# Kernel tuning notes

Measured on AMD Instinct MI355X. Metric: run time of the kernel, lower is better.

## Reference

```python
import jax, jax.numpy as jnp
import numpy as np

FRAME_LEN = 512
FRAME_HOP = 256
EPSILON = float(np.finfo(np.float32).eps)


def _dft_kernels(frame_len=FRAME_LEN):
    # Matches torch: K = view_as_real(fft.rfft(eye(N), dim=1))[:frame_len], windowed by hann.
    # rfft of delta at t gives exp(-2pi i f t / N): real = cos, imag = -sin.
    N = frame_len  # already a power of two
    n = jnp.arange(frame_len, dtype=jnp.float32)
    window = 0.5 * (1.0 - jnp.cos(2.0 * jnp.pi * n / frame_len))  # periodic hann
    f = jnp.arange(N // 2 + 1, dtype=jnp.float32)  # 257 bins
    ang = 2.0 * jnp.pi * f[:, None] * n[None, :] / N  # [F, L]
    Kr = jnp.cos(ang) * window
    Ki = -jnp.sin(ang) * window  # torch rfft imaginary part
    return Kr, Ki


def _frame(x, frame_len=FRAME_LEN, hop=FRAME_HOP):
    B, Ns = x.shape
    T = (Ns - frame_len) // hop + 1
    idx = jnp.arange(T)[:, None] * hop + jnp.arange(frame_len)[None, :]  # [T, L]
    return x[:, idx]  # [B, T, L]


def reference(x):
    Kr, Ki = _dft_kernels()
    xf = _frame(x)  # [B, T, L]
    r = jnp.einsum('btl,fl->bft', xf, Kr)       # real part of conv1d output
    i = -jnp.einsum('btl,fl->bft', xf, Ki)      # i = -imag (as in torch code)
    mag = jnp.sqrt(r * r + i * i)               # B x F x T
    f = jnp.clip(mag, EPSILON, None)
    mean = jnp.mean(f, axis=-1, keepdims=True)
    std = jnp.std(f, axis=-1, keepdims=True, ddof=1)  # torch std is unbiased
    feat = (f - mean) / (std + EPSILON)
    return mag, feat


def setup_inputs() -> dict:
    key = jax.random.key(0)
    x = jax.random.normal(key, (64, 160000), dtype=jnp.float32)
    return {"x": x}
```

## Files before the change

kernel.cpp:

```cpp
#include <hip/hip_runtime.h>
#include <math.h>

#define FRAME_LEN 512
#define HOP       256
#define NFREQ     257
#define NFREQ_PAD 288
#define NBATCH    64
#define NSAMP     160000
#define TFRAMES   624
#define EPS       1.1920928955078125e-07f

#define MT 128
#define FT 32
#define BK 64
#define NK (FRAME_LEN / BK)
#define NXCD 8
#define XBLKS 5000

typedef __attribute__((ext_vector_type(8))) short short8;
typedef __attribute__((ext_vector_type(4))) float f32x4;

static __device__ __forceinline__ unsigned int f2bf(float f) {
    unsigned int u = __float_as_uint(f);
    return (u + 0x7fffu + ((u >> 16) & 1u)) >> 16;
}
static __device__ __forceinline__ uint4 pack8(float4 a, float4 b) {
    uint4 r;
    r.x = f2bf(a.x) | (f2bf(a.y) << 16);
    r.y = f2bf(a.z) | (f2bf(a.w) << 16);
    r.z = f2bf(b.x) | (f2bf(b.y) << 16);
    r.w = f2bf(b.z) | (f2bf(b.w) << 16);
    return r;
}
static __device__ __forceinline__ void gload_lds16(const void* g, void* l) {
    __builtin_amdgcn_global_load_lds(
        (const __attribute__((address_space(1))) void*)g,
        (__attribute__((address_space(3))) void*)l, 16, 0, 0);
}

__global__ __launch_bounds__(256) void prep(const float* __restrict__ x,
                                            unsigned short* __restrict__ xbf,
                                            unsigned short* __restrict__ Wc,
                                            unsigned short* __restrict__ Ws) {
    if (blockIdx.x < XBLKS) {
        int i = blockIdx.x * 256 + threadIdx.x;
        const float4* src = (const float4*)x + (size_t)i * 2;
        float4 a = src[0], b = src[1];
        *(uint4*)(xbf + (size_t)i * 8) = pack8(a, b);
    } else {
        int f = blockIdx.x - XBLKS;
        for (int n = threadIdx.x; n < FRAME_LEN; n += 256) {
            unsigned short c = 0, s = 0;
            if (f < NFREQ) {
                float w = 0.5f * (1.0f - cosf(2.0f * (float)M_PI * (float)n / (float)FRAME_LEN));
                int r = (f * n) & (FRAME_LEN - 1);
                float ang = (float)r * (2.0f * (float)M_PI / (float)FRAME_LEN);
                float sv, cv;
                sincosf(ang, &sv, &cv);
                c = (unsigned short)f2bf(cv * w);
                s = (unsigned short)f2bf(sv * w);
            }
            Wc[f * FRAME_LEN + n] = c;
            Ws[f * FRAME_LEN + n] = s;
        }
    }
}

__global__ __launch_bounds__(256) void stft_mfma(
    const unsigned short* __restrict__ xbf, const unsigned short* __restrict__ Wc,
    const unsigned short* __restrict__ Ws, float* __restrict__ mag)
{
    __shared__ unsigned short As[2][MT][BK];
    __shared__ unsigned short Bs[2][2][FT][BK];

    const int tid = threadIdx.x;
    const int logical = (blockIdx.x % NXCD) * (2808 / NXCD) + blockIdx.x / NXCD;
    const int tileM = logical / 9;
    const int tileF = logical % 9;
    const int wid = tid >> 6;
    const int lane = tid & 63;
    const int lrow = lane & 15;
    const int lhi = lane >> 4;

    const unsigned short* pA[4];
    #pragma unroll
    for (int j = 0; j < 4; j++) {
        int idx = wid * 4 + j;
        int row = idx * 8 + (lane >> 3);
        int m = tileM * MT + row;
        int b = m / TFRAMES;
        int t = m - b * TFRAMES;
        int chunk = (lane & 7) ^ (row & 7);
        pA[j] = xbf + (size_t)b * NSAMP + t * HOP + chunk * 8;
    }
    const unsigned short* pB[2];
    #pragma unroll
    for (int j = 0; j < 2; j++) {
        int i = wid * 2 + j;
        int row = (i & 3) * 8 + (lane >> 3);
        int f = tileF * FT + row;
        int chunk = (lane & 7) ^ (row & 7);
        const unsigned short* tbl = (i & 4) ? Ws : Wc;
        pB[j] = tbl + f * FRAME_LEN + chunk * 8;
    }

    f32x4 accr[2][2] = {};
    f32x4 acci[2][2] = {};

    #pragma unroll
    for (int j = 0; j < 4; j++)
        gload_lds16(pA[j], (unsigned short*)As[0] + (wid * 4 + j) * 512);
    #pragma unroll
    for (int j = 0; j < 2; j++)
        gload_lds16(pB[j], (unsigned short*)Bs[0] + (wid * 2 + j) * 512);
    __syncthreads();

    for (int it = 0; it < NK; it++) {
        const int cur = it & 1;
        if (it < NK - 1) {
            const int k0 = (it + 1) * BK;
            #pragma unroll
            for (int j = 0; j < 4; j++)
                gload_lds16(pA[j] + k0, (unsigned short*)As[cur ^ 1] + (wid * 4 + j) * 512);
            #pragma unroll
            for (int j = 0; j < 2; j++)
                gload_lds16(pB[j] + k0, (unsigned short*)Bs[cur ^ 1] + (wid * 2 + j) * 512);
        }
        #pragma unroll
        for (int ks = 0; ks < 2; ks++) {
            short8 a[2], bc[2], bsn[2];
            const int c = (ks * 4 + lhi) ^ (lrow & 7);
            #pragma unroll
            for (int mf = 0; mf < 2; mf++)
                a[mf] = *(const short8*)&As[cur][wid * 32 + mf * 16 + lrow][c * 8];
            #pragma unroll
            for (int nf = 0; nf < 2; nf++) {
                bc[nf]  = *(const short8*)&Bs[cur][0][nf * 16 + lrow][c * 8];
                bsn[nf] = *(const short8*)&Bs[cur][1][nf * 16 + lrow][c * 8];
            }
            #pragma unroll
            for (int mf = 0; mf < 2; mf++) {
                #pragma unroll
                for (int nf = 0; nf < 2; nf++) {
                    accr[mf][nf] = __builtin_amdgcn_mfma_f32_16x16x32_bf16(
                        a[mf], bc[nf], accr[mf][nf], 0, 0, 0);
                    acci[mf][nf] = __builtin_amdgcn_mfma_f32_16x16x32_bf16(
                        a[mf], bsn[nf], acci[mf][nf], 0, 0, 0);
                }
            }
        }
        __syncthreads();
    }

    #pragma unroll
    for (int mf = 0; mf < 2; mf++) {
        int m0 = tileM * MT + wid * 32 + mf * 16 + lhi * 4;
        int b = m0 / TFRAMES;
        int t = m0 - b * TFRAMES;
        #pragma unroll
        for (int nf = 0; nf < 2; nf++) {
            int f = tileF * FT + nf * 16 + lrow;
            if (f < NFREQ) {
                float4 o;
                o.x = sqrtf(accr[mf][nf][0] * accr[mf][nf][0] + acci[mf][nf][0] * acci[mf][nf][0]);
                o.y = sqrtf(accr[mf][nf][1] * accr[mf][nf][1] + acci[mf][nf][1] * acci[mf][nf][1]);
                o.z = sqrtf(accr[mf][nf][2] * accr[mf][nf][2] + acci[mf][nf][2] * acci[mf][nf][2]);
                o.w = sqrtf(accr[mf][nf][3] * accr[mf][nf][3] + acci[mf][nf][3] * acci[mf][nf][3]);
                *(float4*)(mag + ((size_t)b * NFREQ + f) * TFRAMES + t) = o;
            }
        }
    }
}

__global__ __launch_bounds__(256) void normalize(const float* __restrict__ mag,
                                                 float* __restrict__ feat)
{
    const int row = blockIdx.x * 4 + (threadIdx.x >> 6);
    const int lane = threadIdx.x & 63;
    const float* mp = mag + (size_t)row * TFRAMES;

    float4 v[3];
    float sum = 0.f;
    #pragma unroll
    for (int i = 0; i < 3; i++) {
        int c4 = lane + i * 64;
        if (c4 < TFRAMES / 4) {
            float4 t = *(const float4*)(mp + c4 * 4);
            t.x = fmaxf(t.x, EPS); t.y = fmaxf(t.y, EPS);
            t.z = fmaxf(t.z, EPS); t.w = fmaxf(t.w, EPS);
            v[i] = t;
            sum += (t.x + t.y) + (t.z + t.w);
        } else {
            v[i] = make_float4(0.f, 0.f, 0.f, 0.f);
        }
    }
    #pragma unroll
    for (int off = 1; off < 64; off <<= 1) sum += __shfl_xor(sum, off, 64);
    const float mean = sum * (1.0f / (float)TFRAMES);

    float ssd = 0.f;
    #pragma unroll
    for (int i = 0; i < 3; i++) {
        int c4 = lane + i * 64;
        if (c4 < TFRAMES / 4) {
            float dx = v[i].x - mean, dy = v[i].y - mean;
            float dz = v[i].z - mean, dw = v[i].w - mean;
            ssd += (dx * dx + dy * dy) + (dz * dz + dw * dw);
        }
    }
    #pragma unroll
    for (int off = 1; off < 64; off <<= 1) ssd += __shfl_xor(ssd, off, 64);
    const float stdv = sqrtf(ssd * (1.0f / (float)(TFRAMES - 1)));
    const float inv = 1.0f / (stdv + EPS);

    float* fp = feat + (size_t)row * TFRAMES;
    #pragma unroll
    for (int i = 0; i < 3; i++) {
        int c4 = lane + i * 64;
        if (c4 < TFRAMES / 4) {
            float4 o;
            o.x = (v[i].x - mean) * inv; o.y = (v[i].y - mean) * inv;
            o.z = (v[i].z - mean) * inv; o.w = (v[i].w - mean) * inv;
            *(float4*)(fp + c4 * 4) = o;
        }
    }
}

extern "C" void kernel_launch(void* const* d_in, const int* in_sizes, int n_in,
                              void* d_out, int out_size, void* d_ws, size_t ws_size,
                              hipStream_t stream) {
    const float* x = (const float*)d_in[0];
    unsigned short* Wc  = (unsigned short*)d_ws;
    unsigned short* Ws  = Wc + NFREQ_PAD * FRAME_LEN;
    unsigned short* xbf = Ws + NFREQ_PAD * FRAME_LEN;
    float* mag  = (float*)d_out;
    float* feat = mag + (size_t)NBATCH * NFREQ * TFRAMES;

    prep<<<XBLKS + NFREQ_PAD, 256, 0, stream>>>(x, xbf, Wc, Ws);

    stft_mfma<<<312 * 9, 256, 0, stream>>>(xbf, Wc, Ws, mag);

    normalize<<<NBATCH * NFREQ / 4, 256, 0, stream>>>(mag, feat);
}
```

Before: 61.49 us.

## Fuse STFT magnitude GEMM with per-row normalization using register-stashed values

```diff
diff --git a/kernel.cpp b/kernel.cpp
--- a/kernel.cpp
+++ b/kernel.cpp
@@ -9,13 +9,7 @@
 #define NSAMP     160000
 #define TFRAMES   624
 #define EPS       1.1920928955078125e-07f
-
-#define MT 128
-#define FT 32
-#define BK 64
-#define NK (FRAME_LEN / BK)
-#define NXCD 8
-#define XBLKS 5000
+#define XBLKS     5000
 
 typedef __attribute__((ext_vector_type(8))) short short8;
 typedef __attribute__((ext_vector_type(4))) float f32x4;
@@ -23,6 +17,12 @@
 static __device__ __forceinline__ unsigned int f2bf(float f) {
     unsigned int u = __float_as_uint(f);
     return (u + 0x7fffu + ((u >> 16) & 1u)) >> 16;
+}
+static __device__ __forceinline__ float bf2f_lo(unsigned int p) {
+    return __uint_as_float(p << 16);
+}
+static __device__ __forceinline__ float bf2f_hi(unsigned int p) {
+    return __uint_as_float(p & 0xffff0000u);
 }
 static __device__ __forceinline__ uint4 pack8(float4 a, float4 b) {
     uint4 r;
@@ -66,162 +66,169 @@
     }
 }
 
-__global__ __launch_bounds__(256) void stft_mfma(
-    const unsigned short* __restrict__ xbf, const unsigned short* __restrict__ Wc,
-    const unsigned short* __restrict__ Ws, float* __restrict__ mag)
+static __device__ __forceinline__ void stage(
+    unsigned short* AsB, unsigned short* BsB, int buf, int p, int c,
+    const unsigned short* xb, const unsigned short* Wc, const unsigned short* Ws,
+    int ftile, int tid)
 {
-    __shared__ unsigned short As[2][MT][BK];
-    __shared__ unsigned short Bs[2][2][FT][BK];
-
-    const int tid = threadIdx.x;
-    const int logical = (blockIdx.x % NXCD) * (2808 / NXCD) + blockIdx.x / NXCD;
-    const int tileM = logical / 9;
-    const int tileF = logical % 9;
-    const int wid = tid >> 6;
-    const int lane = tid & 63;
-    const int lrow = lane & 15;
-    const int lhi = lane >> 4;
-
-    const unsigned short* pA[4];
-    #pragma unroll
-    for (int j = 0; j < 4; j++) {
-        int idx = wid * 4 + j;
-        int row = idx * 8 + (lane >> 3);
-        int m = tileM * MT + row;
-        int b = m / TFRAMES;
-        int t = m - b * TFRAMES;
-        int chunk = (lane & 7) ^ (row & 7);
-        pA[j] = xbf + (size_t)b * NSAMP + t * HOP + chunk * 8;
-    }
-    const unsigned short* pB[2];
-    #pragma unroll
-    for (int j = 0; j < 2; j++) {
-        int i = wid * 2 + j;
-        int row = (i & 3) * 8 + (lane >> 3);
-        int f = tileF * FT + row;
-        int chunk = (lane & 7) ^ (row & 7);
-        const unsigned short* tbl = (i & 4) ? Ws : Wc;
-        pB[j] = tbl + f * FRAME_LEN + chunk * 8;
-    }
-
-    f32x4 accr[2][2] = {};
-    f32x4 acci[2][2] = {};
-
+    const int k0 = c * 32;
+    int t = p * 256 + tid;
+    if (t > TFRAMES - 1) t = TFRAMES - 1;
+    const unsigned short* srcA = xb + t * HOP + k0;
     #pragma unroll
     for (int j = 0; j < 4; j++)
-        gload_lds16(pA[j], (unsigned short*)As[0] + (wid * 4 + j) * 512);
-    #pragma unroll
-    for (int j = 0; j < 2; j++)
-        gload_lds16(pB[j], (unsigned short*)Bs[0] + (wid * 2 + j) * 512);
-    __syncthreads();
-
-    for (int it = 0; it < NK; it++) {
-        const int cur = it & 1;
-        if (it < NK - 1) {
-            const int k0 = (it + 1) * BK;
-            #pragma unroll
-            for (int j = 0; j < 4; j++)
-                gload_lds16(pA[j] + k0, (unsigned short*)As[cur ^ 1] + (wid * 4 + j) * 512);
-            #pragma unroll
-            for (int j = 0; j < 2; j++)
-                gload_lds16(pB[j] + k0, (unsigned short*)Bs[cur ^ 1] + (wid * 2 + j) * 512);
-        }
-        #pragma unroll
-        for (int ks = 0; ks < 2; ks++) {
-            short8 a[2], bc[2], bsn[2];
-            const int c = (ks * 4 + lhi) ^ (lrow & 7);
-            #pragma unroll
-            for (int mf = 0; mf < 2; mf++)
-                a[mf] = *(const short8*)&As[cur][wid * 32 + mf * 16 + lrow][c * 8];
+        gload_lds16(srcA + j * 8, AsB + buf * 8192 + j * 2048 + tid * 8);
+    const unsigned short* tb = (tid < 128) ? Wc : Ws;
+    const int bf = ftile * 32 + (tid & 31);
+    const int ch = (tid & 127) >> 5;
+    gload_lds16(tb + bf * 512 + k0 + ch * 8, BsB + buf * 2048 + tid * 8);
+}
+
+template<int P, int MF, int WS>
+static __device__ __forceinline__ void do_pass(
+    int& buf, unsigned short* AsB, unsigned short* BsB,
+    const unsigned short* xb, const unsigned short* Wc, const unsigned short* Ws,
+    int ftile, int tid, int wid, int lrow, int lhi, int b,
+    float* __restrict__ mag, float* ssum, float* ssq,
+    unsigned int stash[10][2][2])
+{
+    f32x4 ar[MF][2] = {};
+    f32x4 ai[MF][2] = {};
+    #pragma unroll
+    for (int c = 0; c < 16; c++) {
+        const int nit = P * 16 + c + 1;
+        if (nit < 48)
+            stage(AsB, BsB, buf ^ 1, nit >> 4, nit & 15, xb, Wc, Ws, ftile, tid);
+        short8 av[MF], bcv[2], bsv[2];
+        #pragma unroll
+        for (int mf = 0; mf < MF; mf++)
+            av[mf] = *(const short8*)(AsB + buf * 8192 + lhi * 2048 +
+                                      (wid * WS + mf * 16 + lrow) * 8);
+        #pragma unroll
+        for (int nf = 0; nf < 2; nf++) {
+            bcv[nf] = *(const short8*)(BsB + buf * 2048 + lhi * 256 + (nf * 16 + lrow) * 8);
+            bsv[nf] = *(const short8*)(BsB + buf * 2048 + 1024 + lhi * 256 + (nf * 16 + lrow) * 8);
+        }
+        #pragma unroll
+        for (int mf = 0; mf < MF; mf++) {
             #pragma unroll
             for (int nf = 0; nf < 2; nf++) {
-                bc[nf]  = *(const short8*)&Bs[cur][0][nf * 16 + lrow][c * 8];
-                bsn[nf] = *(const short8*)&Bs[cur][1][nf * 16 + lrow][c * 8];
-            }
+                ar[mf][nf] = __builtin_amdgcn_mfma_f32_16x16x32_bf16(
+                    av[mf], bcv[nf], ar[mf][nf], 0, 0, 0);
+                ai[mf][nf] = __builtin_amdgcn_mfma_f32_16x16x32_bf16(
+                    av[mf], bsv[nf], ai[mf][nf], 0, 0, 0);
+            }
+        }
+        __syncthreads();
+        buf ^= 1;
+    }
+    #pragma unroll
+    for (int mf = 0; mf < MF; mf++) {
+        const int tile = (P < 2) ? (P * 16 + wid * 4 + mf) : (32 + wid * 2 + mf);
+        const int t = tile * 16 + lhi * 4;
+        const bool tv = (tile < 39);
+        #pragma unroll
+        for (int nf = 0; nf < 2; nf++) {
+            const int f = ftile * 32 + nf * 16 + lrow;
+            const float m0 = sqrtf(ar[mf][nf][0] * ar[mf][nf][0] + ai[mf][nf][0] * ai[mf][nf][0]);
+            const float m1 = sqrtf(ar[mf][nf][1] * ar[mf][nf][1] + ai[mf][nf][1] * ai[mf][nf][1]);
+            const float m2 = sqrtf(ar[mf][nf][2] * ar[mf][nf][2] + ai[mf][nf][2] * ai[mf][nf][2]);
+            const float m3 = sqrtf(ar[mf][nf][3] * ar[mf][nf][3] + ai[mf][nf][3] * ai[mf][nf][3]);
+            if (tv && f < NFREQ) {
+                float4 o = make_float4(m0, m1, m2, m3);
+                *(float4*)(mag + ((size_t)b * NFREQ + f) * TFRAMES + t) = o;
+            }
+            const float c0 = fmaxf(m0, EPS), c1 = fmaxf(m1, EPS);
+            const float c2 = fmaxf(m2, EPS), c3 = fmaxf(m3, EPS);
+            if (tv) {
+                ssum[nf] += (c0 + c1) + (c2 + c3);
+                ssq[nf]  += (c0 * c0 + c1 * c1) + (c2 * c2 + c3 * c3);
+            }
+            const int si = (P < 2) ? (P * 4 + mf) : (8 + mf);
+            stash[si][nf][0] = f2bf(c0) | (f2bf(c1) << 16);
+            stash[si][nf][1] = f2bf(c2) | (f2bf(c3) << 16);
+        }
+    }
+}
+
+__global__ __launch_bounds__(256) void stft_fused(
+    const unsigned short* __restrict__ xbf, const unsigned short* __restrict__ Wc,
+    const unsigned short* __restrict__ Ws, float* __restrict__ mag,
+    float* __restrict__ feat)
+{
+    __shared__ unsigned short As[2][4][256][8];
+    __shared__ unsigned short Bs[2][2][4][32][8];
+    const int tid = threadIdx.x;
+    const int logical = ((int)blockIdx.x & 7) * 72 + ((int)blockIdx.x >> 3);
+    const int b = logical / 9;
+    const int ftile = logical - b * 9;
+    const int wid = tid >> 6, lane = tid & 63, lrow = lane & 15, lhi = lane >> 4;
+    const unsigned short* xb = xbf + (size_t)b * NSAMP;
+    unsigned short* AsB = &As[0][0][0][0];
+    unsigned short* BsB = &Bs[0][0][0][0][0];
+
+    float ssum[2] = {0.f, 0.f}, ssq[2] = {0.f, 0.f};
+    unsigned int stash[10][2][2];
+
+    stage(AsB, BsB, 0, 0, 0, xb, Wc, Ws, ftile, tid);
+    __syncthreads();
+    int buf = 0;
+    do_pass<0, 4, 64>(buf, AsB, BsB, xb, Wc, Ws, ftile, tid, wid, lrow, lhi, b, mag, ssum, ssq, stash);
+    do_pass<1, 4, 64>(buf, AsB, BsB, xb, Wc, Ws, ftile, tid, wid, lrow, lhi, b, mag, ssum, ssq, stash);
+    do_pass<2, 2, 32>(buf, AsB, BsB, xb, Wc, Ws, ftile, tid, wid, lrow, lhi, b, mag, ssum, ssq, stash);
+
+    #pragma unroll
+    for (int nf = 0; nf < 2; nf++) {
+        ssum[nf] += __shfl_xor(ssum[nf], 16, 64);
+        ssum[nf] += __shfl_xor(ssum[nf], 32, 64);
+        ssq[nf]  += __shfl_xor(ssq[nf], 16, 64);
+        ssq[nf]  += __shfl_xor(ssq[nf], 32, 64);
+    }
+    float* red = (float*)AsB;
+    if (lane < 16) {
+        #pragma unroll
+        for (int nf = 0; nf < 2; nf++) {
+            red[((wid * 2 + nf) * 16 + lane) * 2 + 0] = ssum[nf];
+            red[((wid * 2 + nf) * 16 + lane) * 2 + 1] = ssq[nf];
+        }
+    }
+    __syncthreads();
+    float mean[2], inv[2];
+    #pragma unroll
+    for (int nf = 0; nf < 2; nf++) {
+        float S = 0.f, Q = 0.f;
+        #pragma unroll
+        for (int w = 0; w < 4; w++) {
+            S += red[((w * 2 + nf) * 16 + lrow) * 2 + 0];
+            Q += red[((w * 2 + nf) * 16 + lrow) * 2 + 1];
+        }
+        const float mu = S * (1.0f / (float)TFRAMES);
+        float var = (Q - (float)TFRAMES * mu * mu) * (1.0f / (float)(TFRAMES - 1));
+        var = fmaxf(var, 0.f);
+        mean[nf] = mu;
+        inv[nf] = 1.0f / (sqrtf(var) + EPS);
+    }
+    #pragma unroll
+    for (int si = 0; si < 10; si++) {
+        const int tile = (si < 8) ? ((si >> 2) * 16 + wid * 4 + (si & 3))
+                                  : (32 + wid * 2 + (si - 8));
+        const int t = tile * 16 + lhi * 4;
+        if (tile < 39) {
             #pragma unroll
-            for (int mf = 0; mf < 2; mf++) {
-                #pragma unroll
-                for (int nf = 0; nf < 2; nf++) {
-                    accr[mf][nf] = __builtin_amdgcn_mfma_f32_16x16x32_bf16(
-                        a[mf], bc[nf], accr[mf][nf], 0, 0, 0);
-                    acci[mf][nf] = __builtin_amdgcn_mfma_f32_16x16x32_bf16(
-                        a[mf], bsn[nf], acci[mf][nf], 0, 0, 0);
+            for (int nf = 0; nf < 2; nf++) {
+                const int f = ftile * 32 + nf * 16 + lrow;
+                if (f < NFREQ) {
+                    const float c0 = bf2f_lo(stash[si][nf][0]);
+                    const float c1 = bf2f_hi(stash[si][nf][0]);
+                    const float c2 = bf2f_lo(stash[si][nf][1]);
+                    const float c3 = bf2f_hi(stash[si][nf][1]);
+                    float4 o = make_float4((c0 - mean[nf]) * inv[nf],
+                                           (c1 - mean[nf]) * inv[nf],
+                                           (c2 - mean[nf]) * inv[nf],
+                                           (c3 - mean[nf]) * inv[nf]);
+                    *(float4*)(feat + ((size_t)b * NFREQ + f) * TFRAMES + t) = o;
                 }
             }
-        }
-        __syncthreads();
-    }
-
-    #pragma unroll
-    for (int mf = 0; mf < 2; mf++) {
-        int m0 = tileM * MT + wid * 32 + mf * 16 + lhi * 4;
-        int b = m0 / TFRAMES;
-        int t = m0 - b * TFRAMES;
-        #pragma unroll
-        for (int nf = 0; nf < 2; nf++) {
-            int f = tileF * FT + nf * 16 + lrow;
-            if (f < NFREQ) {
-                float4 o;
-                o.x = sqrtf(accr[mf][nf][0] * accr[mf][nf][0] + acci[mf][nf][0] * acci[mf][nf][0]);
-                o.y = sqrtf(accr[mf][nf][1] * accr[mf][nf][1] + acci[mf][nf][1] * acci[mf][nf][1]);
-                o.z = sqrtf(accr[mf][nf][2] * accr[mf][nf][2] + acci[mf][nf][2] * acci[mf][nf][2]);
-                o.w = sqrtf(accr[mf][nf][3] * accr[mf][nf][3] + acci[mf][nf][3] * acci[mf][nf][3]);
-                *(float4*)(mag + ((size_t)b * NFREQ + f) * TFRAMES + t) = o;
-            }
-        }
-    }
-}
-
-__global__ __launch_bounds__(256) void normalize(const float* __restrict__ mag,
-                                                 float* __restrict__ feat)
-{
-    const int row = blockIdx.x * 4 + (threadIdx.x >> 6);
-    const int lane = threadIdx.x & 63;
-    const float* mp = mag + (size_t)row * TFRAMES;
-
-    float4 v[3];
-    float sum = 0.f;
-    #pragma unroll
-    for (int i = 0; i < 3; i++) {
-        int c4 = lane + i * 64;
-        if (c4 < TFRAMES / 4) {
-            float4 t = *(const float4*)(mp + c4 * 4);
-            t.x = fmaxf(t.x, EPS); t.y = fmaxf(t.y, EPS);
-            t.z = fmaxf(t.z, EPS); t.w = fmaxf(t.w, EPS);
-            v[i] = t;
-            sum += (t.x + t.y) + (t.z + t.w);
-        } else {
-            v[i] = make_float4(0.f, 0.f, 0.f, 0.f);
-        }
-    }
-    #pragma unroll
-    for (int off = 1; off < 64; off <<= 1) sum += __shfl_xor(sum, off, 64);
-    const float mean = sum * (1.0f / (float)TFRAMES);
-
-    float ssd = 0.f;
-    #pragma unroll
-    for (int i = 0; i < 3; i++) {
-        int c4 = lane + i * 64;
-        if (c4 < TFRAMES / 4) {
-            float dx = v[i].x - mean, dy = v[i].y - mean;
-            float dz = v[i].z - mean, dw = v[i].w - mean;
-            ssd += (dx * dx + dy * dy) + (dz * dz + dw * dw);
-        }
-    }
-    #pragma unroll
-    for (int off = 1; off < 64; off <<= 1) ssd += __shfl_xor(ssd, off, 64);
-    const float stdv = sqrtf(ssd * (1.0f / (float)(TFRAMES - 1)));
-    const float inv = 1.0f / (stdv + EPS);
-
-    float* fp = feat + (size_t)row * TFRAMES;
-    #pragma unroll
-    for (int i = 0; i < 3; i++) {
-        int c4 = lane + i * 64;
-        if (c4 < TFRAMES / 4) {
-            float4 o;
-            o.x = (v[i].x - mean) * inv; o.y = (v[i].y - mean) * inv;
-            o.z = (v[i].z - mean) * inv; o.w = (v[i].w - mean) * inv;
-            *(float4*)(fp + c4 * 4) = o;
         }
     }
 }
@@ -238,7 +245,5 @@
 
     prep<<<XBLKS + NFREQ_PAD, 256, 0, stream>>>(x, xbf, Wc, Ws);
 
-    stft_mfma<<<312 * 9, 256, 0, stream>>>(xbf, Wc, Ws, mag);
-
-    normalize<<<NBATCH * NFREQ / 4, 256, 0, stream>>>(mag, feat);
-}
+    stft_fused<<<NBATCH * 9, 256, 0, stream>>>(xbf, Wc, Ws, mag, feat);
+}
```

Result: slower. 122.2 us (+98.8%).

## Triple-buffer LDS tiles with partial vmcnt waits in STFT MFMA loop

Applied to the files above, without the earlier changes.

```diff
diff --git a/kernel.cpp b/kernel.cpp
--- a/kernel.cpp
+++ b/kernel.cpp
@@ -16,6 +16,9 @@
 #define NK (FRAME_LEN / BK)
 #define NXCD 8
 #define XBLKS 5000
+
+#define AS (MT * BK)
+#define BS (2 * FT * BK)
 
 typedef __attribute__((ext_vector_type(8))) short short8;
 typedef __attribute__((ext_vector_type(4))) float f32x4;
@@ -70,8 +73,8 @@
     const unsigned short* __restrict__ xbf, const unsigned short* __restrict__ Wc,
     const unsigned short* __restrict__ Ws, float* __restrict__ mag)
 {
-    __shared__ unsigned short As[2][MT][BK];
-    __shared__ unsigned short Bs[2][2][FT][BK];
+    __shared__ unsigned short As[3][MT][BK];
+    __shared__ unsigned short Bs[3][2][FT][BK];
 
     const int tid = threadIdx.x;
     const int logical = (blockIdx.x % NXCD) * (2808 / NXCD) + blockIdx.x / NXCD;
@@ -82,6 +85,9 @@
     const int lrow = lane & 15;
     const int lhi = lane >> 4;
 
+    unsigned short* AsB = &As[0][0][0];
+    unsigned short* BsB = &Bs[0][0][0][0];
+
     const unsigned short* pA[4];
     #pragma unroll
     for (int j = 0; j < 4; j++) {
@@ -108,23 +114,29 @@
     f32x4 acci[2][2] = {};
 
     #pragma unroll
-    for (int j = 0; j < 4; j++)
-        gload_lds16(pA[j], (unsigned short*)As[0] + (wid * 4 + j) * 512);
-    #pragma unroll
-    for (int j = 0; j < 2; j++)
-        gload_lds16(pB[j], (unsigned short*)Bs[0] + (wid * 2 + j) * 512);
-    __syncthreads();
-
+    for (int s = 0; s < 2; s++) {
+        #pragma unroll
+        for (int j = 0; j < 4; j++)
+            gload_lds16(pA[j] + s * BK, AsB + s * AS + (wid * 4 + j) * 512);
+        #pragma unroll
+        for (int j = 0; j < 2; j++)
+            gload_lds16(pB[j] + s * BK, BsB + s * BS + (wid * 2 + j) * 512);
+    }
+    asm volatile("s_waitcnt vmcnt(6)" ::: "memory");
+    __builtin_amdgcn_s_barrier();
+
+    #pragma unroll
     for (int it = 0; it < NK; it++) {
-        const int cur = it & 1;
-        if (it < NK - 1) {
-            const int k0 = (it + 1) * BK;
+        const int cur = it % 3;
+        if (it + 2 < NK) {
+            const int nb = (it + 2) % 3;
+            const int k0 = (it + 2) * BK;
             #pragma unroll
             for (int j = 0; j < 4; j++)
-                gload_lds16(pA[j] + k0, (unsigned short*)As[cur ^ 1] + (wid * 4 + j) * 512);
+                gload_lds16(pA[j] + k0, AsB + nb * AS + (wid * 4 + j) * 512);
             #pragma unroll
             for (int j = 0; j < 2; j++)
-                gload_lds16(pB[j] + k0, (unsigned short*)Bs[cur ^ 1] + (wid * 2 + j) * 512);
+                gload_lds16(pB[j] + k0, BsB + nb * BS + (wid * 2 + j) * 512);
         }
         #pragma unroll
         for (int ks = 0; ks < 2; ks++) {
@@ -132,11 +144,14 @@
             const int c = (ks * 4 + lhi) ^ (lrow & 7);
             #pragma unroll
             for (int mf = 0; mf < 2; mf++)
-                a[mf] = *(const short8*)&As[cur][wid * 32 + mf * 16 + lrow][c * 8];
+                a[mf] = *(const short8*)(AsB + cur * AS +
+                    (wid * 32 + mf * 16 + lrow) * BK + c * 8);
             #pragma unroll
             for (int nf = 0; nf < 2; nf++) {
-                bc[nf]  = *(const short8*)&Bs[cur][0][nf * 16 + lrow][c * 8];
-                bsn[nf] = *(const short8*)&Bs[cur][1][nf * 16 + lrow][c * 8];
+                bc[nf]  = *(const short8*)(BsB + cur * BS +
+                    (nf * 16 + lrow) * BK + c * 8);
+                bsn[nf] = *(const short8*)(BsB + cur * BS + FT * BK +
+                    (nf * 16 + lrow) * BK + c * 8);
             }
             #pragma unroll
             for (int mf = 0; mf < 2; mf++) {
@@ -149,7 +164,11 @@
                 }
             }
         }
-        __syncthreads();
+        if (it < NK - 1) {
+            if (it + 2 < NK) asm volatile("s_waitcnt vmcnt(6)" ::: "memory");
+            else             asm volatile("s_waitcnt vmcnt(0)" ::: "memory");
+            __builtin_amdgcn_s_barrier();
+        }
     }
 
     #pragma unroll
```

After: 64.61 us. 5.1% more time.

## Exploit even/odd sample split and frequency symmetry to halve DFT MFMA work

Applied to the files above, without the earlier changes.

```diff
diff --git a/kernel.cpp b/kernel.cpp
--- a/kernel.cpp
+++ b/kernel.cpp
@@ -4,18 +4,20 @@
 #define FRAME_LEN 512
 #define HOP       256
 #define NFREQ     257
-#define NFREQ_PAD 288
 #define NBATCH    64
 #define NSAMP     160000
+#define NSAMPH    80000
 #define TFRAMES   624
 #define EPS       1.1920928955078125e-07f
 
 #define MT 128
 #define FT 32
 #define BK 64
-#define NK (FRAME_LEN / BK)
-#define NXCD 8
+#define KH 256
 #define XBLKS 5000
+
+#define ASZ (MT * BK)
+#define BSZ (2 * FT * BK)
 
 typedef __attribute__((ext_vector_type(8))) short short8;
 typedef __attribute__((ext_vector_type(4))) float f32x4;
@@ -23,14 +25,6 @@
 static __device__ __forceinline__ unsigned int f2bf(float f) {
     unsigned int u = __float_as_uint(f);
     return (u + 0x7fffu + ((u >> 16) & 1u)) >> 16;
-}
-static __device__ __forceinline__ uint4 pack8(float4 a, float4 b) {
-    uint4 r;
-    r.x = f2bf(a.x) | (f2bf(a.y) << 16);
-    r.y = f2bf(a.z) | (f2bf(a.w) << 16);
-    r.z = f2bf(b.x) | (f2bf(b.y) << 16);
-    r.w = f2bf(b.z) | (f2bf(b.w) << 16);
-    return r;
 }
 static __device__ __forceinline__ void gload_lds16(const void* g, void* l) {
     __builtin_amdgcn_global_load_lds(
@@ -39,50 +33,68 @@
 }
 
 __global__ __launch_bounds__(256) void prep(const float* __restrict__ x,
-                                            unsigned short* __restrict__ xbf,
-                                            unsigned short* __restrict__ Wc,
-                                            unsigned short* __restrict__ Ws) {
+                                            unsigned short* __restrict__ xe,
+                                            unsigned short* __restrict__ xo,
+                                            unsigned short* __restrict__ Wec,
+                                            unsigned short* __restrict__ Wes,
+                                            unsigned short* __restrict__ Woc,
+                                            unsigned short* __restrict__ Wos) {
     if (blockIdx.x < XBLKS) {
         int i = blockIdx.x * 256 + threadIdx.x;
         const float4* src = (const float4*)x + (size_t)i * 2;
         float4 a = src[0], b = src[1];
-        *(uint4*)(xbf + (size_t)i * 8) = pack8(a, b);
+        uint2 e, o;
+        e.x = f2bf(a.x) | (f2bf(a.z) << 16);
+        e.y = f2bf(b.x) | (f2bf(b.z) << 16);
+        o.x = f2bf(a.y) | (f2bf(a.w) << 16);
+        o.y = f2bf(b.y) | (f2bf(b.w) << 16);
+        *(uint2*)(xe + (size_t)i * 4) = e;
+        *(uint2*)(xo + (size_t)i * 4) = o;
     } else {
         int f = blockIdx.x - XBLKS;
-        for (int n = threadIdx.x; n < FRAME_LEN; n += 256) {
-            unsigned short c = 0, s = 0;
-            if (f < NFREQ) {
-                float w = 0.5f * (1.0f - cosf(2.0f * (float)M_PI * (float)n / (float)FRAME_LEN));
-                int r = (f * n) & (FRAME_LEN - 1);
-                float ang = (float)r * (2.0f * (float)M_PI / (float)FRAME_LEN);
-                float sv, cv;
-                sincosf(ang, &sv, &cv);
-                c = (unsigned short)f2bf(cv * w);
-                s = (unsigned short)f2bf(sv * w);
-            }
-            Wc[f * FRAME_LEN + n] = c;
-            Ws[f * FRAME_LEN + n] = s;
-        }
+        int n2 = threadIdx.x;
+        unsigned short ec = 0, es = 0, oc = 0, os = 0;
+        if (f <= 128) {
+            int ne = 2 * n2, no = 2 * n2 + 1;
+            float we = 0.5f * (1.0f - cosf(2.0f * (float)M_PI * (float)ne / (float)FRAME_LEN));
+            float wo = 0.5f * (1.0f - cosf(2.0f * (float)M_PI * (float)no / (float)FRAME_LEN));
+            float ange = (float)((f * ne) & (FRAME_LEN - 1)) * (2.0f * (float)M_PI / (float)FRAME_LEN);
+            float ango = (float)((f * no) & (FRAME_LEN - 1)) * (2.0f * (float)M_PI / (float)FRAME_LEN);
+            float se_, ce_, so_, co_;
+            sincosf(ange, &se_, &ce_);
+            sincosf(ango, &so_, &co_);
+            ec = (unsigned short)f2bf(ce_ * we);
+            es = (unsigned short)f2bf(se_ * we);
+            oc = (unsigned short)f2bf(co_ * wo);
+            os = (unsigned short)f2bf(so_ * wo);
+        }
+        Wec[f * KH + n2] = ec; Wes[f * KH + n2] = es;
+        Woc[f * KH + n2] = oc; Wos[f * KH + n2] = os;
     }
 }
 
 __global__ __launch_bounds__(256) void stft_mfma(
-    const unsigned short* __restrict__ xbf, const unsigned short* __restrict__ Wc,
-    const unsigned short* __restrict__ Ws, float* __restrict__ mag)
+    const unsigned short* __restrict__ xe, const unsigned short* __restrict__ xo,
+    const unsigned short* __restrict__ Wec, const unsigned short* __restrict__ Wes,
+    const unsigned short* __restrict__ Woc, const unsigned short* __restrict__ Wos,
+    float* __restrict__ mag)
 {
     __shared__ unsigned short As[2][MT][BK];
     __shared__ unsigned short Bs[2][2][FT][BK];
 
     const int tid = threadIdx.x;
-    const int logical = (blockIdx.x % NXCD) * (2808 / NXCD) + blockIdx.x / NXCD;
-    const int tileM = logical / 9;
-    const int tileF = logical % 9;
+    const int logical = ((int)blockIdx.x & 7) * 195 + ((int)blockIdx.x >> 3);
+    const int tileM = logical / 5;
+    const int tileF = logical % 5;
     const int wid = tid >> 6;
     const int lane = tid & 63;
     const int lrow = lane & 15;
     const int lhi = lane >> 4;
 
-    const unsigned short* pA[4];
+    unsigned short* AsB = &As[0][0][0];
+    unsigned short* BsB = &Bs[0][0][0][0];
+
+    const unsigned short* pA[2][4];
     #pragma unroll
     for (int j = 0; j < 4; j++) {
         int idx = wid * 4 + j;
@@ -91,40 +103,46 @@
         int b = m / TFRAMES;
         int t = m - b * TFRAMES;
         int chunk = (lane & 7) ^ (row & 7);
-        pA[j] = xbf + (size_t)b * NSAMP + t * HOP + chunk * 8;
-    }
-    const unsigned short* pB[2];
+        size_t off = (size_t)b * NSAMPH + t * (HOP / 2) + chunk * 8;
+        pA[0][j] = xe + off;
+        pA[1][j] = xo + off;
+    }
+    const unsigned short* pB[2][2];
     #pragma unroll
     for (int j = 0; j < 2; j++) {
         int i = wid * 2 + j;
         int row = (i & 3) * 8 + (lane >> 3);
-        int f = tileF * FT + row;
+        int fg = tileF * FT + row;
         int chunk = (lane & 7) ^ (row & 7);
-        const unsigned short* tbl = (i & 4) ? Ws : Wc;
-        pB[j] = tbl + f * FRAME_LEN + chunk * 8;
-    }
-
-    f32x4 accr[2][2] = {};
-    f32x4 acci[2][2] = {};
+        size_t off = (size_t)fg * KH + chunk * 8;
+        pB[0][j] = ((i & 4) ? Wes : Wec) + off;
+        pB[1][j] = ((i & 4) ? Wos : Woc) + off;
+    }
+
+    f32x4 aC[2][2][2] = {};
+    f32x4 aS[2][2][2] = {};
 
     #pragma unroll
     for (int j = 0; j < 4; j++)
-        gload_lds16(pA[j], (unsigned short*)As[0] + (wid * 4 + j) * 512);
+        gload_lds16(pA[0][j], AsB + (wid * 4 + j) * 512);
     #pragma unroll
     for (int j = 0; j < 2; j++)
-        gload_lds16(pB[j], (unsigned short*)Bs[0] + (wid * 2 + j) * 512);
+        gload_lds16(pB[0][j], BsB + (wid * 2 + j) * 512);
     __syncthreads();
 
-    for (int it = 0; it < NK; it++) {
-        const int cur = it & 1;
-        if (it < NK - 1) {
-            const int k0 = (it + 1) * BK;
+    int buf = 0;
+    #pragma unroll
+    for (int it = 0; it < 8; it++) {
+        const int p = it >> 2;
+        if (it < 7) {
+            const int pn = (it + 1) >> 2;
+            const int k0 = ((it + 1) & 3) * BK;
             #pragma unroll
             for (int j = 0; j < 4; j++)
-                gload_lds16(pA[j] + k0, (unsigned short*)As[cur ^ 1] + (wid * 4 + j) * 512);
+                gload_lds16(pA[pn][j] + k0, AsB + (buf ^ 1) * ASZ + (wid * 4 + j) * 512);
             #pragma unroll
             for (int j = 0; j < 2; j++)
-                gload_lds16(pB[j] + k0, (unsigned short*)Bs[cur ^ 1] + (wid * 2 + j) * 512);
+                gload_lds16(pB[pn][j] + k0, BsB + (buf ^ 1) * BSZ + (wid * 2 + j) * 512);
         }
         #pragma unroll
         for (int ks = 0; ks < 2; ks++) {
@@ -132,24 +150,28 @@
             const int c = (ks * 4 + lhi) ^ (lrow & 7);
             #pragma unroll
             for (int mf = 0; mf < 2; mf++)
-                a[mf] = *(const short8*)&As[cur][wid * 32 + mf * 16 + lrow][c * 8];
+                a[mf] = *(const short8*)(AsB + buf * ASZ +
+                    (wid * 32 + mf * 16 + lrow) * BK + c * 8);
             #pragma unroll
             for (int nf = 0; nf < 2; nf++) {
-                bc[nf]  = *(const short8*)&Bs[cur][0][nf * 16 + lrow][c * 8];
-                bsn[nf] = *(const short8*)&Bs[cur][1][nf * 16 + lrow][c * 8];
+                bc[nf]  = *(const short8*)(BsB + buf * BSZ +
+                    (nf * 16 + lrow) * BK + c * 8);
+                bsn[nf] = *(const short8*)(BsB + buf * BSZ + FT * BK +
+                    (nf * 16 + lrow) * BK + c * 8);
             }
             #pragma unroll
             for (int mf = 0; mf < 2; mf++) {
                 #pragma unroll
                 for (int nf = 0; nf < 2; nf++) {
-                    accr[mf][nf] = __builtin_amdgcn_mfma_f32_16x16x32_bf16(
-                        a[mf], bc[nf], accr[mf][nf], 0, 0, 0);
-                    acci[mf][nf] = __builtin_amdgcn_mfma_f32_16x16x32_bf16(
-                        a[mf], bsn[nf], acci[mf][nf], 0, 0, 0);
+                    aC[p][mf][nf] = __builtin_amdgcn_mfma_f32_16x16x32_bf16(
+                        a[mf], bc[nf], aC[p][mf][nf], 0, 0, 0);
+                    aS[p][mf][nf] = __builtin_amdgcn_mfma_f32_16x16x32_bf16(
+                        a[mf], bsn[nf], aS[p][mf][nf], 0, 0, 0);
                 }
             }
         }
         __syncthreads();
+        buf ^= 1;
     }
 
     #pragma unroll
@@ -160,14 +182,20 @@
         #pragma unroll
         for (int nf = 0; nf < 2; nf++) {
             int f = tileF * FT + nf * 16 + lrow;
-            if (f < NFREQ) {
-                float4 o;
-                o.x = sqrtf(accr[mf][nf][0] * accr[mf][nf][0] + acci[mf][nf][0] * acci[mf][nf][0]);
-                o.y = sqrtf(accr[mf][nf][1] * accr[mf][nf][1] + acci[mf][nf][1] * acci[mf][nf][1]);
-                o.z = sqrtf(accr[mf][nf][2] * accr[mf][nf][2] + acci[mf][nf][2] * acci[mf][nf][2]);
-                o.w = sqrtf(accr[mf][nf][3] * accr[mf][nf][3] + acci[mf][nf][3] * acci[mf][nf][3]);
-                *(float4*)(mag + ((size_t)b * NFREQ + f) * TFRAMES + t) = o;
+            float4 od, om;
+            #pragma unroll
+            for (int q = 0; q < 4; q++) {
+                const float Ce = aC[0][mf][nf][q], Co = aC[1][mf][nf][q];
+                const float Se = aS[0][mf][nf][q], So = aS[1][mf][nf][q];
+                const float rd = Ce + Co, id = Se + So;
+                const float rm = Ce - Co, im = So - Se;
+                (&od.x)[q] = sqrtf(rd * rd + id * id);
+                (&om.x)[q] = sqrtf(rm * rm + im * im);
             }
+            if (f <= 128)
+                *(float4*)(mag + ((size_t)b * NFREQ + f) * TFRAMES + t) = od;
+            if (f <= 127)
+                *(float4*)(mag + ((size_t)b * NFREQ + (256 - f)) * TFRAMES + t) = om;
         }
     }
 }
@@ -230,15 +258,18 @@
                               void* d_out, int out_size, void* d_ws, size_t ws_size,
                               hipStream_t stream) {
     const float* x = (const float*)d_in[0];
-    unsigned short* Wc  = (unsigned short*)d_ws;
-    unsigned short* Ws  = Wc + NFREQ_PAD * FRAME_LEN;
-    unsigned short* xbf = Ws + NFREQ_PAD * FRAME_LEN;
+    unsigned short* Wec = (unsigned short*)d_ws;
+    unsigned short* Wes = Wec + 160 * KH;
+    unsigned short* Woc = Wes + 160 * KH;
+    unsigned short* Wos = Woc + 160 * KH;
+    unsigned short* xe  = Wos + 160 * KH;
+    unsigned short* xo  = xe + (size_t)NBATCH * NSAMPH;
     float* mag  = (float*)d_out;
     float* feat = mag + (size_t)NBATCH * NFREQ * TFRAMES;
 
-    prep<<<XBLKS + NFREQ_PAD, 256, 0, stream>>>(x, xbf, Wc, Ws);
-
-    stft_mfma<<<312 * 9, 256, 0, stream>>>(xbf, Wc, Ws, mag);
+    prep<<<XBLKS + 160, 256, 0, stream>>>(x, xe, xo, Wec, Wes, Woc, Wos);
+
+    stft_mfma<<<312 * 5, 256, 0, stream>>>(xe, xo, Wec, Wes, Woc, Wos, mag);
 
     normalize<<<NBATCH * NFREQ / 4, 256, 0, stream>>>(mag, feat);
 }
```

Result: faster. 54.40 us (-11.5%).
